# Kernel tuning notes

Measured on AMD Instinct MI355X. Metric: run time of the kernel, lower is better.

The kernel has to match this reference:

```python
import jax, jax.numpy as jnp
import numpy as np

B, N, C_IN, C_OUT, CHEB_K, EMBED = 64, 2048, 64, 64, 3, 16

def setup_inputs() -> dict:
    key = jax.random.key(0)
    k1, k2, k3, k4 = jax.random.split(key, 4)
    x = jax.random.normal(k1, (B, N, C_IN), dtype=jnp.float32)
    node_embedding = jax.random.normal(k2, (N, EMBED), dtype=jnp.float32)
    weights_pool = jax.random.normal(k3, (EMBED, CHEB_K, C_IN, C_OUT), dtype=jnp.float32) * 0.1
    bias_pool = jax.random.normal(k4, (EMBED, C_OUT), dtype=jnp.float32) * 0.1
    return {"x": x, "node_embedding": node_embedding,
            "weights_pool": weights_pool, "bias_pool": bias_pool}

def reference(x, node_embedding, weights_pool, bias_pool):
    cheb_k = weights_pool.shape[1]
    n = node_embedding.shape[0]
    # adaptive adjacency: softmax over rows of relu(E @ E^T)
    support = jax.nn.softmax(jax.nn.relu(node_embedding @ node_embedding.T), axis=1)
    # Chebyshev recursion: T0 = I, T1 = support, Tk = 2*support@Tk-1 - Tk-2
    supports = [jnp.eye(n, dtype=support.dtype), support]
    for _ in range(2, cheb_k):
        supports.append(2.0 * support @ supports[-1] - supports[-2])
    supports = jnp.stack(supports, axis=0)  # (K, N, N)
    # per-node weights/bias generated from embedding
    weights = jnp.einsum('nd,dkio->nkio', node_embedding, weights_pool)  # (N,K,Cin,Cout)
    bias = node_embedding @ bias_pool  # (N, Cout)
    # graph conv: gather K-hop features then per-node grouped matmul
    x_g = jnp.einsum('knm,bmc->bnkc', supports, x)  # (B,N,K,Cin)
    x_gconv = jnp.einsum('bnki,nkio->bno', x_g, weights) + bias
    return x_gconv
```

## Files before the change

kernel.cpp:

```cpp
#include <hip/hip_runtime.h>
#include <math.h>

#define NN    2048
#define BATCH 64
#define CIN   64
#define COUT  64
#define EMB   16
#define JDIM  4096
#define WKI   192

typedef __bf16 bf16_t;
typedef __bf16 bf16x8 __attribute__((ext_vector_type(8)));
typedef float  f32x4  __attribute__((ext_vector_type(4)));
typedef unsigned int u32x4 __attribute__((ext_vector_type(4)));

#define GLOAD16(gp, lp) __builtin_amdgcn_global_load_lds( \
    (const __attribute__((address_space(1))) void*)(gp),  \
    (__attribute__((address_space(3))) void*)(lp), 16, 0, 0)

static __device__ __forceinline__ unsigned short bfbits(float f) {
    return __builtin_bit_cast(unsigned short, (bf16_t)f);
}

__global__ __launch_bounds__(256) void wgen_kernel(
    const float* __restrict__ E, const float* __restrict__ wp,
    bf16_t* __restrict__ Wt) {
    __shared__ float wL[3072 * 4];
    __shared__ float sE[32][16];
    const int s  = blockIdx.x % 24;
    const int n0 = (blockIdx.x / 24) * 32;
    const int t  = threadIdx.x;
    const int oki0 = s * 512 + 2 * t;
    const int o = oki0 / WKI, r0 = oki0 % WKI;
    const int o_lo = (s * 512) / WKI;

    if (t < 128) {
        const int node = t >> 2, q = t & 3;
        *reinterpret_cast<float4*>(&sE[node][q * 4]) =
            *reinterpret_cast<const float4*>(E + (size_t)(n0 + node) * EMB + q * 4);
    }
    {
        const int oo  = t & 3;
        const int col = min(o_lo + oo, 63);
#pragma unroll
        for (int i = 0; i < 48; ++i) {
            int dr = (t >> 2) + i * 64;
            wL[dr * 4 + oo] = wp[(size_t)dr * 64 + col];
        }
    }
    __syncthreads();

    float w[2][EMB];
#pragma unroll
    for (int d = 0; d < EMB; ++d) {
        w[0][d] = wL[(d * WKI + r0) * 4 + (o - o_lo)];
        w[1][d] = wL[(d * WKI + r0 + 1) * 4 + (o - o_lo)];
    }

#pragma unroll 2
    for (int nn = 0; nn < 32; ++nn) {
        float4 e0 = *reinterpret_cast<const float4*>(&sE[nn][0]);
        float4 e1 = *reinterpret_cast<const float4*>(&sE[nn][4]);
        float4 e2 = *reinterpret_cast<const float4*>(&sE[nn][8]);
        float4 e3 = *reinterpret_cast<const float4*>(&sE[nn][12]);
        float en[EMB] = {e0.x,e0.y,e0.z,e0.w, e1.x,e1.y,e1.z,e1.w,
                         e2.x,e2.y,e2.z,e2.w, e3.x,e3.y,e3.z,e3.w};
        float a0 = 0.f, a1 = 0.f;
#pragma unroll
        for (int d = 0; d < EMB; ++d) {
            a0 += en[d] * w[0][d];
            a1 += en[d] * w[1][d];
        }
        unsigned int pk = (unsigned int)bfbits(a0) | ((unsigned int)bfbits(a1) << 16);
        __builtin_nontemporal_store(pk,
            reinterpret_cast<unsigned int*>(Wt + (size_t)(n0 + nn) * 12288 + oki0));
    }
}

__global__ __launch_bounds__(256) void sy_kernel(
    const float* __restrict__ x, const float* __restrict__ E,
    bf16_t* __restrict__ Y0, bf16_t* __restrict__ Sb) {
    __shared__ float smem[64 * 65];
    const int bid = blockIdx.x;
    const int tid = threadIdx.x;

    if (bid < 2048) {
        float* vals = smem;
        float* red  = smem + 2048;
        const int n = bid;

        float en[EMB];
#pragma unroll
        for (int d = 0; d < EMB; ++d) en[d] = E[n * EMB + d];

        float lmax = -1e30f;
        for (int m = tid; m < NN; m += 256) {
            const float4* em = reinterpret_cast<const float4*>(E + m * EMB);
            float dot = 0.f;
#pragma unroll
            for (int q = 0; q < EMB / 4; ++q) {
                float4 v = em[q];
                dot += en[q*4+0]*v.x + en[q*4+1]*v.y + en[q*4+2]*v.z + en[q*4+3]*v.w;
            }
            float r = fmaxf(dot, 0.f);
            vals[m] = r;
            lmax = fmaxf(lmax, r);
        }
#pragma unroll
        for (int off = 32; off > 0; off >>= 1)
            lmax = fmaxf(lmax, __shfl_down(lmax, off, 64));
        if ((tid & 63) == 0) red[tid >> 6] = lmax;
        __syncthreads();
        const float gmax = fmaxf(fmaxf(red[0], red[1]), fmaxf(red[2], red[3]));
        __syncthreads();

        float lsum = 0.f;
        for (int m = tid; m < NN; m += 256) {
            float e = expf(vals[m] - gmax);
            vals[m] = e;
            lsum += e;
        }
#pragma unroll
        for (int off = 32; off > 0; off >>= 1)
            lsum += __shfl_down(lsum, off, 64);
        if ((tid & 63) == 0) red[tid >> 6] = lsum;
        __syncthreads();
        const float inv = 1.f / (red[0] + red[1] + red[2] + red[3]);

        for (int m = tid; m < NN; m += 256)
            Sb[(size_t)n * NN + m] = (bf16_t)(vals[m] * inv);
    } else {
        float (*tile)[65] = reinterpret_cast<float(*)[65]>(smem);
        const int yb = bid - 2048;
        const int n0 = (yb & 31) * 64, b = yb >> 5;
        const int c = tid & 63, nn0 = tid >> 6;
        const float* src = x + ((size_t)b * NN + n0) * CIN + c;
#pragma unroll
        for (int p = 0; p < 16; ++p) {
            int nn = nn0 + p * 4;
            tile[nn][c] = src[(size_t)nn * CIN];
        }
        __syncthreads();
        const int cc = tid >> 2, q = tid & 3;
        bf16_t* dst = Y0 + (size_t)(b * 64 + cc) * NN + n0 + q * 16;
#pragma unroll
        for (int s4 = 0; s4 < 4; ++s4) {
            ushort4 pk;
            pk.x = bfbits(tile[q * 16 + s4 * 4 + 0][cc]);
            pk.y = bfbits(tile[q * 16 + s4 * 4 + 1][cc]);
            pk.z = bfbits(tile[q * 16 + s4 * 4 + 2][cc]);
            pk.w = bfbits(tile[q * 16 + s4 * 4 + 3][cc]);
            *reinterpret_cast<ushort4*>(dst + s4 * 4) = pk;
        }
    }
}

template<int MODE>
__global__ __launch_bounds__(256) void gemm_bt(
    const bf16_t* __restrict__ A, const bf16_t* __restrict__ Bt,
    bf16_t* __restrict__ Cj, bf16_t* __restrict__ GT) {
    __shared__ bf16_t smem[128 * 136];
    bf16_t* As = smem;
    bf16_t* Bs = smem + 4096;
    bf16_t* T  = smem;
    const int tid  = threadIdx.x;
    const int wave = tid >> 6, lane = tid & 63;
    const int pBlk = blockIdx.x * 128;
    const int mBlk = blockIdx.y * 128;
    const int K = NN;

    const bf16_t* aSrc = A  + (size_t)(mBlk + wave * 32 + (lane >> 2)) * K + (lane & 3) * 8;
    const bf16_t* bSrc = Bt + (size_t)(pBlk + wave * 32 + (lane >> 2)) * K + (lane & 3) * 8;
    bf16_t* aDst = As + wave * 1024;
    bf16_t* bDst = Bs + wave * 1024;

    f32x4 acc[4][4] = {};
    const int wr = wave >> 1, wc = wave & 1;
    const int lrow = lane & 15, lk = (lane >> 4) * 8;

    for (int k0 = 0; k0 < K; k0 += 32) {
        GLOAD16(aSrc + k0,                  aDst);
        GLOAD16(aSrc + k0 + (size_t)16 * K, aDst + 512);
        GLOAD16(bSrc + k0,                  bDst);
        GLOAD16(bSrc + k0 + (size_t)16 * K, bDst + 512);
        __syncthreads();

        bf16x8 af[4], bb[4];
#pragma unroll
        for (int mf = 0; mf < 4; ++mf)
            af[mf] = *reinterpret_cast<const bf16x8*>(
                &As[(wr * 64 + mf * 16 + lrow) * 32 + lk]);
#pragma unroll
        for (int nf = 0; nf < 4; ++nf)
            bb[nf] = *reinterpret_cast<const bf16x8*>(
                &Bs[(wc * 64 + nf * 16 + lrow) * 32 + lk]);
#pragma unroll
        for (int mf = 0; mf < 4; ++mf)
#pragma unroll
            for (int nf = 0; nf < 4; ++nf)
                acc[mf][nf] = __builtin_amdgcn_mfma_f32_16x16x32_bf16(
                    af[mf], bb[nf], acc[mf][nf], 0, 0, 0);
        __syncthreads();
    }

    const int orow = (lane >> 4) * 4, ocol = lane & 15;
    if (MODE == 0) {
#pragma unroll
        for (int mf = 0; mf < 4; ++mf)
#pragma unroll
            for (int nf = 0; nf < 4; ++nf)
#pragma unroll
                for (int r = 0; r < 4; ++r) {
                    size_t row = (size_t)(mBlk + wr * 64 + mf * 16 + orow + r);
                    size_t col = (size_t)(pBlk + wc * 64 + nf * 16 + ocol);
                    Cj[row * NN + col] = (bf16_t)acc[mf][nf][r];
                }
    }
    const float scale = (MODE == 1) ? 2.f : 1.f;
#pragma unroll
    for (int mf = 0; mf < 4; ++mf)
#pragma unroll
        for (int nf = 0; nf < 4; ++nf)
#pragma unroll
            for (int r = 0; r < 4; ++r) {
                int trow = wr * 64 + mf * 16 + orow + r;
                int tcol = wc * 64 + nf * 16 + ocol;
                T[(size_t)tcol * 136 + trow] = (bf16_t)(scale * acc[mf][nf][r]);
            }
    __syncthreads();
    {
        const int row = tid >> 1, half = tid & 1;
        const bf16_t* src = T + (size_t)row * 136 + half * 64;
        bf16_t* dst = GT + (size_t)(pBlk + row) * JDIM + mBlk + half * 64;
#pragma unroll
        for (int s = 0; s < 8; ++s)
            *reinterpret_cast<uint4*>(dst + s * 8) =
                *reinterpret_cast<const uint4*>(src + s * 8);
    }
}

__global__ __launch_bounds__(256) void gconv_kernel(
    const float* __restrict__ x,   const float* __restrict__ E,
    const float* __restrict__ bp,  const bf16_t* __restrict__ G1T,
    const bf16_t* __restrict__ G2T, const bf16_t* __restrict__ Wt,
    float* __restrict__ out) {
    __shared__ bf16_t g[64][200];
    const int n = blockIdx.x;
    const int tid = threadIdx.x, wave = tid >> 6, lane = tid & 63;
    const int lrow = lane & 15, lk = (lane >> 4) * 8;
    const int o = wave * 16 + lrow;

    const bf16_t* wtn = Wt + (size_t)n * 12288 + (size_t)o * WKI;
    bf16x8 bb[6];
#pragma unroll
    for (int ks = 0; ks < 6; ++ks)
        bb[ks] = __builtin_bit_cast(bf16x8, __builtin_nontemporal_load(
            reinterpret_cast<const u32x4*>(wtn + ks * 32 + lk)));
    float bo = 0.f;
    {
        const float* en = E + (size_t)n * EMB;
#pragma unroll
        for (int d = 0; d < EMB; ++d) bo += en[d] * bp[d * COUT + o];
    }

#pragma unroll
    for (int p = 0; p < 2; ++p) {
        int idx = p * 256 + tid;
        int b = idx >> 3, ic = (idx & 7) * 8;
        const float4* xs = reinterpret_cast<const float4*>(
            x + ((size_t)b * NN + n) * CIN + ic);
        float4 x0 = xs[0], x1 = xs[1];
        uint4 g1v = *reinterpret_cast<const uint4*>(G1T + (size_t)n * JDIM + idx * 8);
        uint4 g2v = *reinterpret_cast<const uint4*>(G2T + (size_t)n * JDIM + idx * 8);
        float xv[8] = {x0.x, x0.y, x0.z, x0.w, x1.x, x1.y, x1.z, x1.w};
        const bf16_t* g2p = reinterpret_cast<const bf16_t*>(&g2v);
        ushort4 g0b[2], g2b[2];
#pragma unroll
        for (int e = 0; e < 8; ++e) {
            ((unsigned short*)g0b)[e] = bfbits(xv[e]);
            ((unsigned short*)g2b)[e] = bfbits((float)g2p[e] - xv[e]);
        }
        *reinterpret_cast<uint4*>(&g[b][ic])       = *reinterpret_cast<uint4*>(g0b);
        *reinterpret_cast<uint4*>(&g[b][64 + ic])  = g1v;
        *reinterpret_cast<uint4*>(&g[b][128 + ic]) = *reinterpret_cast<uint4*>(g2b);
    }
    __syncthreads();

    f32x4 acc[4] = {};
#pragma unroll
    for (int ks = 0; ks < 6; ++ks)
#pragma unroll
        for (int mf = 0; mf < 4; ++mf) {
            bf16x8 af = *reinterpret_cast<const bf16x8*>(&g[mf * 16 + lrow][ks * 32 + lk]);
            acc[mf] = __builtin_amdgcn_mfma_f32_16x16x32_bf16(af, bb[ks], acc[mf], 0, 0, 0);
        }
#pragma unroll
    for (int mf = 0; mf < 4; ++mf)
#pragma unroll
        for (int r = 0; r < 4; ++r) {
            int b = mf * 16 + (lane >> 4) * 4 + r;
            __builtin_nontemporal_store(acc[mf][r] + bo,
                &out[((size_t)b * NN + n) * COUT + o]);
        }
}

extern "C" void kernel_launch(void* const* d_in, const int* in_sizes, int n_in,
                              void* d_out, int out_size, void* d_ws, size_t ws_size,
                              hipStream_t stream) {
    const float* x  = (const float*)d_in[0];
    const float* E  = (const float*)d_in[1];
    const float* wp = (const float*)d_in[2];
    const float* bp = (const float*)d_in[3];
    float* out = (float*)d_out;

    bf16_t* ws = (bf16_t*)d_ws;
    bf16_t* Wt  = ws;
    bf16_t* Sb  = Wt + (size_t)NN * 12288;
    bf16_t* Y0  = Sb + (size_t)NN * NN;
    bf16_t* Y1  = Y0 + (size_t)JDIM * NN;
    bf16_t* G1T = Y1 + (size_t)JDIM * NN;
    bf16_t* G2T = Y0;

    sy_kernel<<<4096, 256, 0, stream>>>(x, E, Y0, Sb);
    wgen_kernel<<<24 * 64, 256, 0, stream>>>(E, wp, Wt);

    dim3 ggrid(NN / 128, JDIM / 128);
    gemm_bt<0><<<ggrid, 256, 0, stream>>>(Y0, Sb, Y1, G1T);
    gemm_bt<1><<<ggrid, 256, 0, stream>>>(Y1, Sb, nullptr, G2T);

    gconv_kernel<<<NN, 256, 0, stream>>>(x, E, bp, G1T, G2T, Wt, out);
}
```

Measured before the change: 263.5 us.

## Fuse weight-generation into first GEMM launch as extra blocks

Merges the per-node weight generation kernel into the first Chebyshev GEMM launch: blocks 0-511 run the GEMM tile and the rest run weight generation, so the two independent workloads overlap on the GPU and one launch is saved. Shared memory is sized for the larger of the two roles, which may reduce occupancy for the GEMM blocks. It also replaces the nontemporal load of Wt in the gconv kernel with a plain vector load.

```diff
diff --git a/kernel.cpp b/kernel.cpp
--- a/kernel.cpp
+++ b/kernel.cpp
@@ -12,7 +12,6 @@
 typedef __bf16 bf16_t;
 typedef __bf16 bf16x8 __attribute__((ext_vector_type(8)));
 typedef float  f32x4  __attribute__((ext_vector_type(4)));
-typedef unsigned int u32x4 __attribute__((ext_vector_type(4)));
 
 #define GLOAD16(gp, lp) __builtin_amdgcn_global_load_lds( \
     (const __attribute__((address_space(1))) void*)(gp),  \
@@ -20,61 +19,6 @@
 
 static __device__ __forceinline__ unsigned short bfbits(float f) {
     return __builtin_bit_cast(unsigned short, (bf16_t)f);
-}
-
-__global__ __launch_bounds__(256) void wgen_kernel(
-    const float* __restrict__ E, const float* __restrict__ wp,
-    bf16_t* __restrict__ Wt) {
-    __shared__ float wL[3072 * 4];
-    __shared__ float sE[32][16];
-    const int s  = blockIdx.x % 24;
-    const int n0 = (blockIdx.x / 24) * 32;
-    const int t  = threadIdx.x;
-    const int oki0 = s * 512 + 2 * t;
-    const int o = oki0 / WKI, r0 = oki0 % WKI;
-    const int o_lo = (s * 512) / WKI;
-
-    if (t < 128) {
-        const int node = t >> 2, q = t & 3;
-        *reinterpret_cast<float4*>(&sE[node][q * 4]) =
-            *reinterpret_cast<const float4*>(E + (size_t)(n0 + node) * EMB + q * 4);
-    }
-    {
-        const int oo  = t & 3;
-        const int col = min(o_lo + oo, 63);
-#pragma unroll
-        for (int i = 0; i < 48; ++i) {
-            int dr = (t >> 2) + i * 64;
-            wL[dr * 4 + oo] = wp[(size_t)dr * 64 + col];
-        }
-    }
-    __syncthreads();
-
-    float w[2][EMB];
-#pragma unroll
-    for (int d = 0; d < EMB; ++d) {
-        w[0][d] = wL[(d * WKI + r0) * 4 + (o - o_lo)];
-        w[1][d] = wL[(d * WKI + r0 + 1) * 4 + (o - o_lo)];
-    }
-
-#pragma unroll 2
-    for (int nn = 0; nn < 32; ++nn) {
-        float4 e0 = *reinterpret_cast<const float4*>(&sE[nn][0]);
-        float4 e1 = *reinterpret_cast<const float4*>(&sE[nn][4]);
-        float4 e2 = *reinterpret_cast<const float4*>(&sE[nn][8]);
-        float4 e3 = *reinterpret_cast<const float4*>(&sE[nn][12]);
-        float en[EMB] = {e0.x,e0.y,e0.z,e0.w, e1.x,e1.y,e1.z,e1.w,
-                         e2.x,e2.y,e2.z,e2.w, e3.x,e3.y,e3.z,e3.w};
-        float a0 = 0.f, a1 = 0.f;
-#pragma unroll
-        for (int d = 0; d < EMB; ++d) {
-            a0 += en[d] * w[0][d];
-            a1 += en[d] * w[1][d];
-        }
-        unsigned int pk = (unsigned int)bfbits(a0) | ((unsigned int)bfbits(a1) << 16);
-        __builtin_nontemporal_store(pk,
-            reinterpret_cast<unsigned int*>(Wt + (size_t)(n0 + nn) * 12288 + oki0));
-    }
 }
 
 __global__ __launch_bounds__(256) void sy_kernel(
@@ -151,6 +95,143 @@
             pk.z = bfbits(tile[q * 16 + s4 * 4 + 2][cc]);
             pk.w = bfbits(tile[q * 16 + s4 * 4 + 3][cc]);
             *reinterpret_cast<ushort4*>(dst + s4 * 4) = pk;
+        }
+    }
+}
+
+__global__ __launch_bounds__(256) void gemm0_wgen_kernel(
+    const bf16_t* __restrict__ A, const bf16_t* __restrict__ Bt,
+    bf16_t* __restrict__ Cj, bf16_t* __restrict__ GT,
+    const float* __restrict__ E, const float* __restrict__ wp,
+    bf16_t* __restrict__ Wt) {
+    __shared__ float smemF[12800];
+    const int bid = blockIdx.x;
+    const int tid = threadIdx.x;
+
+    if (bid < 512) {
+        bf16_t* As = reinterpret_cast<bf16_t*>(smemF);
+        bf16_t* Bs = As + 4096;
+        bf16_t* T  = As;
+        const int wave = tid >> 6, lane = tid & 63;
+        const int pBlk = (bid & 15) * 128;
+        const int mBlk = (bid >> 4) * 128;
+        const int K = NN;
+
+        const bf16_t* aSrc = A  + (size_t)(mBlk + wave * 32 + (lane >> 2)) * K + (lane & 3) * 8;
+        const bf16_t* bSrc = Bt + (size_t)(pBlk + wave * 32 + (lane >> 2)) * K + (lane & 3) * 8;
+        bf16_t* aDst = As + wave * 1024;
+        bf16_t* bDst = Bs + wave * 1024;
+
+        f32x4 acc[4][4] = {};
+        const int wr = wave >> 1, wc = wave & 1;
+        const int lrow = lane & 15, lk = (lane >> 4) * 8;
+
+        for (int k0 = 0; k0 < K; k0 += 32) {
+            GLOAD16(aSrc + k0,                  aDst);
+            GLOAD16(aSrc + k0 + (size_t)16 * K, aDst + 512);
+            GLOAD16(bSrc + k0,                  bDst);
+            GLOAD16(bSrc + k0 + (size_t)16 * K, bDst + 512);
+            __syncthreads();
+
+            bf16x8 af[4], bb[4];
+#pragma unroll
+            for (int mf = 0; mf < 4; ++mf)
+                af[mf] = *reinterpret_cast<const bf16x8*>(
+                    &As[(wr * 64 + mf * 16 + lrow) * 32 + lk]);
+#pragma unroll
+            for (int nf = 0; nf < 4; ++nf)
+                bb[nf] = *reinterpret_cast<const bf16x8*>(
+                    &Bs[(wc * 64 + nf * 16 + lrow) * 32 + lk]);
+#pragma unroll
+            for (int mf = 0; mf < 4; ++mf)
+#pragma unroll
+                for (int nf = 0; nf < 4; ++nf)
+                    acc[mf][nf] = __builtin_amdgcn_mfma_f32_16x16x32_bf16(
+                        af[mf], bb[nf], acc[mf][nf], 0, 0, 0);
+            __syncthreads();
+        }
+
+        const int orow = (lane >> 4) * 4, ocol = lane & 15;
+#pragma unroll
+        for (int mf = 0; mf < 4; ++mf)
+#pragma unroll
+            for (int nf = 0; nf < 4; ++nf)
+#pragma unroll
+                for (int r = 0; r < 4; ++r) {
+                    size_t row = (size_t)(mBlk + wr * 64 + mf * 16 + orow + r);
+                    size_t col = (size_t)(pBlk + wc * 64 + nf * 16 + ocol);
+                    Cj[row * NN + col] = (bf16_t)acc[mf][nf][r];
+                }
+#pragma unroll
+        for (int mf = 0; mf < 4; ++mf)
+#pragma unroll
+            for (int nf = 0; nf < 4; ++nf)
+#pragma unroll
+                for (int r = 0; r < 4; ++r) {
+                    int trow = wr * 64 + mf * 16 + orow + r;
+                    int tcol = wc * 64 + nf * 16 + ocol;
+                    T[(size_t)tcol * 136 + trow] = (bf16_t)acc[mf][nf][r];
+                }
+        __syncthreads();
+        {
+            const int row = tid >> 1, half = tid & 1;
+            const bf16_t* src = T + (size_t)row * 136 + half * 64;
+            bf16_t* dst = GT + (size_t)(pBlk + row) * JDIM + mBlk + half * 64;
+#pragma unroll
+            for (int s = 0; s < 8; ++s)
+                *reinterpret_cast<uint4*>(dst + s * 8) =
+                    *reinterpret_cast<const uint4*>(src + s * 8);
+        }
+    } else {
+        float* wL = smemF;
+        float (*sE)[16] = reinterpret_cast<float(*)[16]>(smemF + 12288);
+        const int wb = bid - 512;
+        const int s  = wb % 24;
+        const int n0 = (wb / 24) * 32;
+        const int oki0 = s * 512 + 2 * tid;
+        const int o = oki0 / WKI, r0 = oki0 % WKI;
+        const int o_lo = (s * 512) / WKI;
+
+        if (tid < 128) {
+            const int node = tid >> 2, q = tid & 3;
+            *reinterpret_cast<float4*>(&sE[node][q * 4]) =
+                *reinterpret_cast<const float4*>(E + (size_t)(n0 + node) * EMB + q * 4);
+        }
+        {
+            const int oo  = tid & 3;
+            const int col = min(o_lo + oo, 63);
+#pragma unroll
+            for (int i = 0; i < 48; ++i) {
+                int dr = (tid >> 2) + i * 64;
+                wL[dr * 4 + oo] = wp[(size_t)dr * 64 + col];
+            }
+        }
+        __syncthreads();
+
+        float w[2][EMB];
+#pragma unroll
+        for (int d = 0; d < EMB; ++d) {
+            w[0][d] = wL[(d * WKI + r0) * 4 + (o - o_lo)];
+            w[1][d] = wL[(d * WKI + r0 + 1) * 4 + (o - o_lo)];
+        }
+
+#pragma unroll 2
+        for (int nn = 0; nn < 32; ++nn) {
+            float4 e0 = *reinterpret_cast<const float4*>(&sE[nn][0]);
+            float4 e1 = *reinterpret_cast<const float4*>(&sE[nn][4]);
+            float4 e2 = *reinterpret_cast<const float4*>(&sE[nn][8]);
+            float4 e3 = *reinterpret_cast<const float4*>(&sE[nn][12]);
+            float en[EMB] = {e0.x,e0.y,e0.z,e0.w, e1.x,e1.y,e1.z,e1.w,
+                             e2.x,e2.y,e2.z,e2.w, e3.x,e3.y,e3.z,e3.w};
+            float a0 = 0.f, a1 = 0.f;
+#pragma unroll
+            for (int d = 0; d < EMB; ++d) {
+                a0 += en[d] * w[0][d];
+                a1 += en[d] * w[1][d];
+            }
+            unsigned int pk = (unsigned int)bfbits(a0) | ((unsigned int)bfbits(a1) << 16);
+            __builtin_nontemporal_store(pk,
+                reinterpret_cast<unsigned int*>(Wt + (size_t)(n0 + nn) * 12288 + oki0));
         }
     }
 }
@@ -254,8 +335,7 @@
     bf16x8 bb[6];
 #pragma unroll
     for (int ks = 0; ks < 6; ++ks)
-        bb[ks] = __builtin_bit_cast(bf16x8, __builtin_nontemporal_load(
-            reinterpret_cast<const u32x4*>(wtn + ks * 32 + lk)));
+        bb[ks] = *reinterpret_cast<const bf16x8*>(wtn + ks * 32 + lk);
     float bo = 0.f;
     {
         const float* en = E + (size_t)n * EMB;
@@ -322,10 +402,10 @@
     bf16_t* G2T = Y0;
 
     sy_kernel<<<4096, 256, 0, stream>>>(x, E, Y0, Sb);
-    wgen_kernel<<<24 * 64, 256, 0, stream>>>(E, wp, Wt);
+
+    gemm0_wgen_kernel<<<2048, 256, 0, stream>>>(Y0, Sb, Y1, G1T, E, wp, Wt);
 
     dim3 ggrid(NN / 128, JDIM / 128);
-    gemm_bt<0><<<ggrid, 256, 0, stream>>>(Y0, Sb, Y1, G1T);
     gemm_bt<1><<<ggrid, 256, 0, stream>>>(Y1, Sb, nullptr, G2T);
 
     gconv_kernel<<<NN, 256, 0, stream>>>(x, E, bp, G1T, G2T, Wt, out);
```

Measured after the change: 253.9 us. -3.6%, faster.

## Merge softmax, transpose and weight-generation kernels into one prelude launch

Applied to the files above, without the earlier changes.

Folds the weight-generation kernel into the support/transpose kernel as a third block range, so one launch covers all three jobs. The weight-pool staging is split into two phases so it fits the shared buffer, and that costs extra barriers. The transpose tile stride in the GEMM epilogue goes from 136 to 138, which changes the LDS bank mapping. The gconv weight loads also switch from nontemporal to ordinary loads.

```diff
diff --git a/kernel.cpp b/kernel.cpp
--- a/kernel.cpp
+++ b/kernel.cpp
@@ -8,11 +8,11 @@
 #define EMB   16
 #define JDIM  4096
 #define WKI   192
+#define TPAD  138
 
 typedef __bf16 bf16_t;
 typedef __bf16 bf16x8 __attribute__((ext_vector_type(8)));
 typedef float  f32x4  __attribute__((ext_vector_type(4)));
-typedef unsigned int u32x4 __attribute__((ext_vector_type(4)));
 
 #define GLOAD16(gp, lp) __builtin_amdgcn_global_load_lds( \
     (const __attribute__((address_space(1))) void*)(gp),  \
@@ -22,65 +22,11 @@
     return __builtin_bit_cast(unsigned short, (bf16_t)f);
 }
 
-__global__ __launch_bounds__(256) void wgen_kernel(
-    const float* __restrict__ E, const float* __restrict__ wp,
-    bf16_t* __restrict__ Wt) {
-    __shared__ float wL[3072 * 4];
-    __shared__ float sE[32][16];
-    const int s  = blockIdx.x % 24;
-    const int n0 = (blockIdx.x / 24) * 32;
-    const int t  = threadIdx.x;
-    const int oki0 = s * 512 + 2 * t;
-    const int o = oki0 / WKI, r0 = oki0 % WKI;
-    const int o_lo = (s * 512) / WKI;
-
-    if (t < 128) {
-        const int node = t >> 2, q = t & 3;
-        *reinterpret_cast<float4*>(&sE[node][q * 4]) =
-            *reinterpret_cast<const float4*>(E + (size_t)(n0 + node) * EMB + q * 4);
-    }
-    {
-        const int oo  = t & 3;
-        const int col = min(o_lo + oo, 63);
-#pragma unroll
-        for (int i = 0; i < 48; ++i) {
-            int dr = (t >> 2) + i * 64;
-            wL[dr * 4 + oo] = wp[(size_t)dr * 64 + col];
-        }
-    }
-    __syncthreads();
-
-    float w[2][EMB];
-#pragma unroll
-    for (int d = 0; d < EMB; ++d) {
-        w[0][d] = wL[(d * WKI + r0) * 4 + (o - o_lo)];
-        w[1][d] = wL[(d * WKI + r0 + 1) * 4 + (o - o_lo)];
-    }
-
-#pragma unroll 2
-    for (int nn = 0; nn < 32; ++nn) {
-        float4 e0 = *reinterpret_cast<const float4*>(&sE[nn][0]);
-        float4 e1 = *reinterpret_cast<const float4*>(&sE[nn][4]);
-        float4 e2 = *reinterpret_cast<const float4*>(&sE[nn][8]);
-        float4 e3 = *reinterpret_cast<const float4*>(&sE[nn][12]);
-        float en[EMB] = {e0.x,e0.y,e0.z,e0.w, e1.x,e1.y,e1.z,e1.w,
-                         e2.x,e2.y,e2.z,e2.w, e3.x,e3.y,e3.z,e3.w};
-        float a0 = 0.f, a1 = 0.f;
-#pragma unroll
-        for (int d = 0; d < EMB; ++d) {
-            a0 += en[d] * w[0][d];
-            a1 += en[d] * w[1][d];
-        }
-        unsigned int pk = (unsigned int)bfbits(a0) | ((unsigned int)bfbits(a1) << 16);
-        __builtin_nontemporal_store(pk,
-            reinterpret_cast<unsigned int*>(Wt + (size_t)(n0 + nn) * 12288 + oki0));
-    }
-}
-
-__global__ __launch_bounds__(256) void sy_kernel(
-    const float* __restrict__ x, const float* __restrict__ E,
-    bf16_t* __restrict__ Y0, bf16_t* __restrict__ Sb) {
-    __shared__ float smem[64 * 65];
+__global__ __launch_bounds__(256) void prelude_kernel(
+    const float* __restrict__ x,  const float* __restrict__ E,
+    const float* __restrict__ wp, bf16_t* __restrict__ Y0,
+    bf16_t* __restrict__ Sb,      bf16_t* __restrict__ Wt) {
+    __shared__ float smem[6656];
     const int bid = blockIdx.x;
     const int tid = threadIdx.x;
 
@@ -129,7 +75,7 @@
 
         for (int m = tid; m < NN; m += 256)
             Sb[(size_t)n * NN + m] = (bf16_t)(vals[m] * inv);
-    } else {
+    } else if (bid < 4096) {
         float (*tile)[65] = reinterpret_cast<float(*)[65]>(smem);
         const int yb = bid - 2048;
         const int n0 = (yb & 31) * 64, b = yb >> 5;
@@ -152,6 +98,62 @@
             pk.w = bfbits(tile[q * 16 + s4 * 4 + 3][cc]);
             *reinterpret_cast<ushort4*>(dst + s4 * 4) = pk;
         }
+    } else {
+        float* wL = smem;
+        float (*sE)[16] = reinterpret_cast<float(*)[16]>(smem + 6144);
+        const int wb = bid - 4096;
+        const int s  = wb % 24;
+        const int n0 = (wb / 24) * 32;
+        const int oki0 = s * 512 + 2 * tid;
+        const int o = oki0 / WKI, r0 = oki0 % WKI;
+        const int o_lo = (s * 512) / WKI;
+        const int oo_sel = o - o_lo;
+        const int col = min(o_lo + (tid & 3), 63);
+
+        if (tid < 128) {
+            const int node = tid >> 2, q = tid & 3;
+            *reinterpret_cast<float4*>(&sE[node][q * 4]) =
+                *reinterpret_cast<const float4*>(E + (size_t)(n0 + node) * EMB + q * 4);
+        }
+
+        float w[2][EMB];
+#pragma unroll
+        for (int ph = 0; ph < 2; ++ph) {
+            {
+                const int oo = tid & 3;
+#pragma unroll
+                for (int i = 0; i < 24; ++i) {
+                    int drl = (tid >> 2) + i * 64;
+                    wL[drl * 4 + oo] = wp[(size_t)(ph * 1536 + drl) * 64 + col];
+                }
+            }
+            __syncthreads();
+#pragma unroll
+            for (int dh = 0; dh < 8; ++dh) {
+                w[0][ph * 8 + dh] = wL[(dh * WKI + r0) * 4 + oo_sel];
+                w[1][ph * 8 + dh] = wL[(dh * WKI + r0 + 1) * 4 + oo_sel];
+            }
+            __syncthreads();
+        }
+
+#pragma unroll 2
+        for (int nn = 0; nn < 32; ++nn) {
+            float4 e0 = *reinterpret_cast<const float4*>(&sE[nn][0]);
+            float4 e1 = *reinterpret_cast<const float4*>(&sE[nn][4]);
+            float4 e2 = *reinterpret_cast<const float4*>(&sE[nn][8]);
+            float4 e3 = *reinterpret_cast<const float4*>(&sE[nn][12]);
+            float en[EMB] = {e0.x,e0.y,e0.z,e0.w, e1.x,e1.y,e1.z,e1.w,
+                             e2.x,e2.y,e2.z,e2.w, e3.x,e3.y,e3.z,e3.w};
+            float a0 = 0.f, a1 = 0.f;
+#pragma unroll
+            for (int d = 0; d < EMB; ++d) {
+                a0 += en[d] * w[0][d];
+                a1 += en[d] * w[1][d];
+            }
+            unsigned int pk = (unsigned int)bfbits(a0) | ((unsigned int)bfbits(a1) << 16);
+            __builtin_nontemporal_store(pk,
+                reinterpret_cast<unsigned int*>(Wt + (size_t)(n0 + nn) * 12288 + oki0));
+        }
     }
 }
 
@@ -159,7 +161,7 @@
 __global__ __launch_bounds__(256) void gemm_bt(
     const bf16_t* __restrict__ A, const bf16_t* __restrict__ Bt,
     bf16_t* __restrict__ Cj, bf16_t* __restrict__ GT) {
-    __shared__ bf16_t smem[128 * 136];
+    __shared__ bf16_t smem[128 * TPAD];
     bf16_t* As = smem;
     bf16_t* Bs = smem + 4096;
     bf16_t* T  = smem;
@@ -225,12 +227,12 @@
             for (int r = 0; r < 4; ++r) {
                 int trow = wr * 64 + mf * 16 + orow + r;
                 int tcol = wc * 64 + nf * 16 + ocol;
-                T[(size_t)tcol * 136 + trow] = (bf16_t)(scale * acc[mf][nf][r]);
+                T[(size_t)tcol * TPAD + trow] = (bf16_t)(scale * acc[mf][nf][r]);
             }
     __syncthreads();
     {
         const int row = tid >> 1, half = tid & 1;
-        const bf16_t* src = T + (size_t)row * 136 + half * 64;
+        const bf16_t* src = T + (size_t)row * TPAD + half * 64;
         bf16_t* dst = GT + (size_t)(pBlk + row) * JDIM + mBlk + half * 64;
 #pragma unroll
         for (int s = 0; s < 8; ++s)
@@ -254,8 +256,7 @@
     bf16x8 bb[6];
 #pragma unroll
     for (int ks = 0; ks < 6; ++ks)
-        bb[ks] = __builtin_bit_cast(bf16x8, __builtin_nontemporal_load(
-            reinterpret_cast<const u32x4*>(wtn + ks * 32 + lk)));
+        bb[ks] = *reinterpret_cast<const bf16x8*>(wtn + ks * 32 + lk);
     float bo = 0.f;
     {
         const float* en = E + (size_t)n * EMB;
@@ -321,8 +322,7 @@
     bf16_t* G1T = Y1 + (size_t)JDIM * NN;
     bf16_t* G2T = Y0;
 
-    sy_kernel<<<4096, 256, 0, stream>>>(x, E, Y0, Sb);
-    wgen_kernel<<<24 * 64, 256, 0, stream>>>(E, wp, Wt);
+    prelude_kernel<<<5632, 256, 0, stream>>>(x, E, wp, Y0, Sb, Wt);
 
     dim3 ggrid(NN / 128, JDIM / 128);
     gemm_bt<0><<<ggrid, 256, 0, stream>>>(Y0, Sb, Y1, G1T);
```

New measurement: 260.2 us. No clear change (-1.2%).
